# Performance work log

Hardware: AMD Instinct MI355X
Metric: run time of the kernel (lower is better)

The kernel has to match this reference:

```python
import jax, jax.numpy as jnp
import numpy as np

S = 8        # parallel streams (encoder/decoder pairs)
T_ENC = 12   # encoder timesteps per stream
H = 256      # hidden size
F = 316      # input features
B = 1024     # batch
MAX_LEN = 48
SCALE = 1.0 / np.sqrt(H).astype(np.float32)  # MHA single-head scaling


def _lstm_gates_to_hc(gates, c):
    # PyTorch gate order: i, f, g, o
    i, f, g, o = jnp.split(gates, 4, axis=-1)
    c_new = jax.nn.sigmoid(f) * c + jax.nn.sigmoid(i) * jnp.tanh(g)
    h_new = jax.nn.sigmoid(o) * jnp.tanh(c_new)
    return h_new, c_new


def setup_inputs() -> dict:
    key = jax.random.key(0)
    ks = jax.random.split(key, 20)
    w = 0.05
    inp = {
        'x': jax.random.normal(ks[0], (B, 96, F), jnp.float32),
        'tgt': jax.random.normal(ks[1], (B, MAX_LEN), jnp.float32),
        # encoder LSTM (per-stream stacked): input F -> H
        'W_ih_e': jax.random.normal(ks[2], (S, 4 * H, F), jnp.float32) * w,
        'W_hh_e': jax.random.normal(ks[3], (S, 4 * H, H), jnp.float32) * w,
        'b_ih_e': jnp.zeros((S, 4 * H), jnp.float32),
        'b_hh_e': jnp.zeros((S, 4 * H), jnp.float32),
        # decoder LSTM: input 1 -> H
        'W_ih_d': jax.random.normal(ks[4], (S, 4 * H, 1), jnp.float32) * w,
        'W_hh_d': jax.random.normal(ks[5], (S, 4 * H, H), jnp.float32) * w,
        'b_ih_d': jnp.zeros((S, 4 * H), jnp.float32),
        'b_hh_d': jnp.zeros((S, 4 * H), jnp.float32),
        # MultiheadAttention: in_proj [3H,H] per stream, out_proj [H,H]
        'W_in_attn': jax.random.normal(ks[6], (S, 3 * H, H), jnp.float32) * w,
        'b_in_attn': jnp.zeros((S, 3 * H), jnp.float32),
        'W_out_attn': jax.random.normal(ks[7], (S, H, H), jnp.float32) * w,
        'b_out_attn': jnp.zeros((S, H), jnp.float32),
        # decoder out_fc: 2H -> 1
        'W_fcout': jax.random.normal(ks[8], (S, 1, 2 * H), jnp.float32) * w,
        'b_fcout': jnp.zeros((S, 1), jnp.float32),
        # final fc: 8 -> 1
        'W_fc': jax.random.normal(ks[9], (1, S), jnp.float32) * w,
        'b_fc': jnp.zeros((1,), jnp.float32),
    }
    return inp


def _forward(x, tgt, W_ih_e, W_hh_e, b_ih_e, b_hh_e,
             W_ih_d, W_hh_d, b_ih_d, b_hh_d,
             W_in_attn, b_in_attn, W_out_attn, b_out_attn,
             W_fcout, b_fcout, W_fc, b_fc):
    batch, max_len = x.shape[0], tgt.shape[1]
    # time-major then split 96 steps into 8 streams of 12: [S, T_ENC, B, F]
    xe = x.transpose(1, 0, 2).reshape(S, T_ENC, batch, F)

    # ---- encoders: batched LSTM over 8 streams ----
    def enc_step(carry, xt):  # xt [S,B,F]
        h, c = carry
        gates = (jnp.einsum('sbf,sgf->sbg', xt, W_ih_e) + b_ih_e[:, None, :]
                 + jnp.einsum('sbh,sgh->sbg', h, W_hh_e) + b_hh_e[:, None, :])
        h, c = _lstm_gates_to_hc(gates, c)
        return (h, c), h

    h0 = jnp.zeros((S, batch, H), x.dtype)
    (hT, cT), enc_out = jax.lax.scan(enc_step, (h0, h0), xe.transpose(1, 0, 2, 3))
    # enc_out: [T_ENC, S, B, H]; (hT, cT) seed the decoder hidden state

    # ---- precompute attention K,V ----
    Wq, Wk, Wv = jnp.split(W_in_attn, 3, axis=1)  # each [S,H,H]
    bq, bk, bv = jnp.split(b_in_attn, 3, axis=1)  # each [S,H]
    k = jnp.einsum('tsbh,seh->tsbe', enc_out, Wk) + bk[None, :, None, :]
    v = jnp.einsum('tsbh,seh->tsbe', enc_out, Wv) + bv[None, :, None, :]

    # teacher-forced decoder inputs: step 0 uses x[-1,:,0], step t uses tgt[:,t-1]
    inputs = jnp.concatenate([x[:, -1, 0][None, :], tgt.T[:-1]], axis=0)  # [L,B]

    def dec_step(carry, inp):  # inp [B]
        h, c = carry
        it = jnp.broadcast_to(inp[None, :, None], (S, h.shape[1], 1))
        gates = (jnp.einsum('sbi,sgi->sbg', it, W_ih_d) + b_ih_d[:, None, :]
                 + jnp.einsum('sbh,sgh->sbg', h, W_hh_d) + b_hh_d[:, None, :])
        h, c = _lstm_gates_to_hc(gates, c)
        # single-query MHA (1 head) against encoder outputs
        q = jnp.einsum('sbh,seh->sbe', h, Wq) + bq[:, None, :]
        scores = jnp.einsum('sbe,tsbe->sbt', q, k) * SCALE
        attn = jax.nn.softmax(scores, axis=-1)
        ctx = jnp.einsum('sbt,tsbe->sbe', attn, v)
        ctx = jnp.einsum('sbe,soe->sbo', ctx, W_out_attn) + b_out_attn[:, None, :]
        cat = jnp.concatenate([h, ctx], axis=-1)  # [S,B,2H]
        out = jnp.einsum('sbk,sok->sbo', cat, W_fcout) + b_fcout[:, None, :]
        return (h, c), out[..., 0]  # [S,B]

    _, outs = jax.lax.scan(dec_step, (hT, cT), inputs)  # [L,S,B]
    final = outs.transpose(0, 2, 1)                      # [L,B,S]
    y = jnp.einsum('lbs,os->lbo', final, W_fc) + b_fc    # [L,B,1]
    return y[..., 0].T                                    # [B,L]


def reference(x, tgt, W_ih_e, W_hh_e, b_ih_e, b_hh_e,
              W_ih_d, W_hh_d, b_ih_d, b_hh_d,
              W_in_attn, b_in_attn, W_out_attn, b_out_attn,
              W_fcout, b_fcout, W_fc, b_fc):
    return _forward(x, tgt, W_ih_e, W_hh_e, b_ih_e, b_hh_e,
                    W_ih_d, W_hh_d, b_ih_d, b_hh_d,
                    W_in_attn, b_in_attn, W_out_attn, b_out_attn,
                    W_fcout, b_fcout, W_fc, b_fc)
```

## Files before the change

### kernel.cpp

```cpp
#include <hip/hip_runtime.h>
#include <cstdio>
#include <cstdint>

#define S8     8
#define TENC   12
#define HDIM   256
#define FDIM   316
#define BATCH  1024
#define LDEC   48
#define DBT    32
#define KA     264
#define SCALE_ATTN 0.0625f

typedef short bf16x8 __attribute__((ext_vector_type(8)));
typedef float f32x4  __attribute__((ext_vector_type(4)));

__device__ __forceinline__ float sigf(float x) { return 1.0f / (1.0f + expf(-x)); }

__device__ __forceinline__ unsigned short f2bf(float f) {
  unsigned u = __builtin_bit_cast(unsigned, f);
  unsigned r = (u + 0x7fffu + ((u >> 16) & 1u)) >> 16;
  return (unsigned short)r;
}
__device__ __forceinline__ float bflo(unsigned u) {
  return __builtin_bit_cast(float, u << 16);
}
__device__ __forceinline__ float bfhi(unsigned u) {
  return __builtin_bit_cast(float, u & 0xffff0000u);
}

#define MFMA(acc, a, b) acc = __builtin_amdgcn_mfma_f32_16x16x32_bf16(a, b, acc, 0, 0, 0)

#define DOT8(a, q, hp) \
  a = fmaf(bflo(q.x), hp[0], a); a = fmaf(bfhi(q.x), hp[1], a); \
  a = fmaf(bflo(q.y), hp[2], a); a = fmaf(bfhi(q.y), hp[3], a); \
  a = fmaf(bflo(q.z), hp[4], a); a = fmaf(bfhi(q.z), hp[5], a); \
  a = fmaf(bflo(q.w), hp[6], a); a = fmaf(bfhi(q.w), hp[7], a);

#define UNPS(dst, off, q) \
  dst[off+0] = bflo(q.x); dst[off+1] = bfhi(q.x); \
  dst[off+2] = bflo(q.y); dst[off+3] = bfhi(q.y); \
  dst[off+4] = bflo(q.z); dst[off+5] = bfhi(q.z); \
  dst[off+6] = bflo(q.w); dst[off+7] = bfhi(q.w);

__global__ __launch_bounds__(256) void transpose_k(const float* __restrict__ in,
                                                   float* __restrict__ out,
                                                   int R, int C) {
  __shared__ float tile[32][33];
  const int s = blockIdx.z;
  const size_t base = (size_t)s * R * C;
  const int r0 = blockIdx.y * 32, c0 = blockIdx.x * 32;
  const int tx = threadIdx.x & 31, ty = threadIdx.x >> 5;
  for (int i = ty; i < 32; i += 8) {
    int r = r0 + i, c = c0 + tx;
    if (r < R && c < C) tile[i][tx] = in[base + (size_t)r * C + c];
  }
  __syncthreads();
  for (int i = ty; i < 32; i += 8) {
    int c = c0 + i, r = r0 + tx;
    if (c < C && r < R) out[base + (size_t)c * R + r] = tile[tx][i];
  }
}

__global__ __launch_bounds__(256) void fold_gemm(const float* __restrict__ A, size_t sA,
                                                 const float* __restrict__ Bm, size_t sB,
                                                 float* __restrict__ out, size_t sO) {
  const int s = blockIdx.y, r0 = blockIdx.x * 32, col = threadIdx.x;
  A += (size_t)s * sA; Bm += (size_t)s * sB; out += (size_t)s * sO;
  float acc[32] = {};
  for (int e = 0; e < HDIM; ++e) {
    const float bvv = Bm[(size_t)e * HDIM + col];
#pragma unroll
    for (int r = 0; r < 32; ++r) acc[r] = fmaf(A[(size_t)e * HDIM + r0 + r], bvv, acc[r]);
  }
  for (int r = 0; r < 32; ++r) out[(size_t)(r0 + r) * HDIM + col] = acc[r];
}

__global__ __launch_bounds__(64) void pack_hl(const float* __restrict__ src, int Ksrc, int ksT,
                                              bf16x8* __restrict__ outhi,
                                              bf16x8* __restrict__ outlo) {
  const int s = blockIdx.z, ks = blockIdx.y, nt = blockIdx.x;
  const int lane = threadIdx.x, l15 = lane & 15, quad = lane >> 4;
  const int n = nt * 16 + l15, kb = ks * 32 + quad * 8;
  const float* row = src + ((size_t)s * 1024 + n) * Ksrc;
  union { bf16x8 v; unsigned short e[8]; } h, l;
#pragma unroll
  for (int j = 0; j < 8; ++j) {
    const int k = kb + j;
    const float v = (k < Ksrc) ? row[k] : 0.f;
    const unsigned short hi = f2bf(v);
    h.e[j] = hi;
    l.e[j] = f2bf(v - bflo(hi));
  }
  const size_t idx = (((size_t)s * ksT + ks) * 64 + nt) * 64 + lane;
  outhi[idx] = h.v;
  outlo[idx] = l.v;
}

__global__ __launch_bounds__(64) void pack_s(const float* __restrict__ src, int ntOff,
                                             bf16x8* __restrict__ out) {
  const int s = blockIdx.z, ks = blockIdx.y, nt = blockIdx.x;
  const int lane = threadIdx.x, l15 = lane & 15, quad = lane >> 4;
  const int n = nt * 16 + l15, kb = ks * 32 + quad * 8;
  const float* row = src + ((size_t)s * 256 + n) * 256;
  union { bf16x8 v; unsigned short e[8]; } h;
#pragma unroll
  for (int j = 0; j < 8; ++j) h.e[j] = f2bf(row[kb + j]);
  out[(((size_t)s * 8 + ks) * 32 + ntOff + nt) * 64 + lane] = h.v;
}

__global__ __launch_bounds__(256) void fold_vec2(const float* __restrict__ Win,
                                                 const float* __restrict__ bin,
                                                 const float* __restrict__ Wout,
                                                 const float* __restrict__ bout,
                                                 float* __restrict__ kbv,
                                                 float* __restrict__ cbias) {
  const int s = blockIdx.x, t = threadIdx.x;
  const float* bq = bin + s * 768;
  const float* bv = bin + s * 768 + 512;
  float a0 = 0.f, a1 = 0.f;
  for (int e = 0; e < 256; ++e) {
    a0 = fmaf(Win[((size_t)s * 768 + 256 + e) * 256 + t], bq[e], a0);
    a1 = fmaf(Wout[((size_t)s * 256 + t) * 256 + e], bv[e], a1);
  }
  kbv[s * 256 + t] = a0;
  cbias[s * 256 + t] = a1 + bout[s * 256 + t];
}

__global__ __launch_bounds__(256) void fold_mvw(const float* __restrict__ Mv,
                                                const float* __restrict__ Wfo,
                                                float* __restrict__ mvw) {
  const int s = blockIdx.x, k = threadIdx.x;
  float a = 0.f;
  for (int o = 0; o < 256; ++o)
    a = fmaf(Wfo[s * 512 + 256 + o], Mv[((size_t)s * 256 + o) * 256 + k], a);
  mvw[s * 256 + k] = a;
}

__global__ void fold_bias(const float* __restrict__ a, const float* __restrict__ b,
                          float* __restrict__ o, int n) {
  int i = blockIdx.x * 256 + threadIdx.x;
  if (i < n) o[i] = a[i] + b[i];
}

__global__ void build_decin(const float* __restrict__ x, const float* __restrict__ tgt,
                            float* __restrict__ dec_in) {
  int idx = blockIdx.x * 256 + threadIdx.x;
  if (idx >= LDEC * BATCH) return;
  int l = idx >> 10, b = idx & 1023;
  dec_in[idx] = (l == 0) ? x[(size_t)b * 96 * FDIM + 95 * FDIM]
                         : tgt[(size_t)b * LDEC + (l - 1)];
}

__global__ __launch_bounds__(512) void rec_phase(
    const float* __restrict__ x,
    const bf16x8* __restrict__ WxH, const bf16x8* __restrict__ WxL,
    const bf16x8* __restrict__ WeH, const bf16x8* __restrict__ WeL,
    const bf16x8* __restrict__ WdH, const bf16x8* __restrict__ WdL,
    const float* __restrict__ be, const float* __restrict__ bd,
    const float* __restrict__ wihd, const float* __restrict__ Wfo,
    const float* __restrict__ decin,
    unsigned* __restrict__ hEnc,
    unsigned short* __restrict__ hDec,
    float* __restrict__ hdPart)
{
  __shared__ unsigned short hAhi[DBT * KA];
  __shared__ unsigned short hAlo[DBT * KA];
  __shared__ float beS[1024];
  __shared__ float bdS[1024];
  __shared__ float wdS[1024];
  __shared__ float wfoS[256];
  __shared__ float scrR[DBT * 8];

  const int bid = blockIdx.x;
  const int s = bid & 7, b0 = (bid >> 3) * DBT;
  const int tid = threadIdx.x;
  const int w = tid >> 6, lane = tid & 63, l15 = lane & 15, quad = lane >> 4;

  for (int i = tid; i < DBT * KA; i += 512) { hAhi[i] = 0; hAlo[i] = 0; }
  for (int i = tid; i < 1024; i += 512) {
    beS[i] = be[s * 1024 + i];
    bdS[i] = bd[s * 1024 + i];
    wdS[i] = wihd[s * 1024 + i];
  }
  if (tid < 256) wfoS[tid] = Wfo[s * 512 + tid];

  float cst[2][2][4];
#pragma unroll
  for (int a = 0; a < 2; ++a)
#pragma unroll
    for (int b = 0; b < 2; ++b)
#pragma unroll
      for (int r = 0; r < 4; ++r) cst[a][b][r] = 0.f;

  const bf16x8* wxh = WxH + (size_t)s * 10 * 64 * 64;
  const bf16x8* wxl = WxL + (size_t)s * 10 * 64 * 64;
  const bf16x8* weh = WeH + (size_t)s * 8 * 64 * 64;
  const bf16x8* wel = WeL + (size_t)s * 8 * 64 * 64;
  const bf16x8* wdh = WdH + (size_t)s * 8 * 64 * 64;
  const bf16x8* wdl = WdL + (size_t)s * 8 * 64 * 64;

  __syncthreads();

  for (int t = 0; t < TENC; ++t) {
    f32x4 acc[2][2][4];
#pragma unroll
    for (int mt = 0; mt < 2; ++mt)
#pragma unroll
      for (int st = 0; st < 2; ++st)
#pragma unroll
        for (int c = 0; c < 4; ++c) acc[mt][st][c] = (f32x4){0.f, 0.f, 0.f, 0.f};

    const size_t xoff = (size_t)(s * TENC + t) * FDIM;
    for (int ks = 0; ks < 10; ++ks) {
      bf16x8 axh[2], axl[2];
#pragma unroll
      for (int mt = 0; mt < 2; ++mt) {
        const f32x4* xr = (const f32x4*)(x + (size_t)(b0 + 16 * mt + l15) * (96 * FDIM)
                                         + xoff + ks * 32 + quad * 8);
        const f32x4 v0 = __builtin_nontemporal_load(xr);
        f32x4 v1;
        if (ks == 9 && quad == 3) v1 = (f32x4){0.f, 0.f, 0.f, 0.f};
        else v1 = __builtin_nontemporal_load(xr + 1);
        float vv[8];
#pragma unroll
        for (int j = 0; j < 4; ++j) { vv[j] = v0[j]; vv[4 + j] = v1[j]; }
        union { bf16x8 v; unsigned short e[8]; } uh, ul;
#pragma unroll
        for (int j = 0; j < 8; ++j) {
          const unsigned short hi = f2bf(vv[j]);
          uh.e[j] = hi;
          ul.e[j] = f2bf(vv[j] - bflo(hi));
        }
        axh[mt] = uh.v; axl[mt] = ul.v;
      }
#pragma unroll
      for (int st = 0; st < 2; ++st)
#pragma unroll
        for (int c = 0; c < 4; ++c) {
          const int nt = c * 16 + 2 * w + st;
          const bf16x8 bh = wxh[(ks * 64 + nt) * 64 + lane];
          const bf16x8 bl = wxl[(ks * 64 + nt) * 64 + lane];
          MFMA(acc[0][st][c], axh[0], bh); MFMA(acc[0][st][c], axh[0], bl); MFMA(acc[0][st][c], axl[0], bh);
          MFMA(acc[1][st][c], axh[1], bh); MFMA(acc[1][st][c], axh[1], bl); MFMA(acc[1][st][c], axl[1], bh);
        }
    }
#pragma unroll 2
    for (int ks = 0; ks < 8; ++ks) {
      bf16x8 ah[2], al[2];
#pragma unroll
      for (int mt = 0; mt < 2; ++mt) {
        const int ao = (16 * mt + l15) * KA + ks * 32 + quad * 8;
        ah[mt] = *(const bf16x8*)&hAhi[ao];
        al[mt] = *(const bf16x8*)&hAlo[ao];
      }
#pragma unroll
      for (int st = 0; st < 2; ++st)
#pragma unroll
        for (int c = 0; c < 4; ++c) {
          const int nt = c * 16 + 2 * w + st;
          const bf16x8 bh = weh[(ks * 64 + nt) * 64 + lane];
          const bf16x8 bl = wel[(ks * 64 + nt) * 64 + lane];
          MFMA(acc[0][st][c], ah[0], bh); MFMA(acc[0][st][c], ah[0], bl); MFMA(acc[0][st][c], al[0], bh);
          MFMA(acc[1][st][c], ah[1], bh); MFMA(acc[1][st][c], ah[1], bl); MFMA(acc[1][st][c], al[1], bh);
        }
    }
    float hv[2][2][4];
#pragma unroll
    for (int st = 0; st < 2; ++st) {
      const int J0 = 32 * w + 16 * st + l15;
      const float g0 = beS[J0];
      const float g1 = beS[256 + J0];
      const float g2 = beS[512 + J0];
      const float g3 = beS[768 + J0];
#pragma unroll
      for (int mt = 0; mt < 2; ++mt)
#pragma unroll
        for (int reg = 0; reg < 4; ++reg) {
          const float gi = sigf(acc[mt][st][0][reg] + g0);
          const float gf = sigf(acc[mt][st][1][reg] + g1);
          const float gg = tanhf(acc[mt][st][2][reg] + g2);
          const float go = sigf(acc[mt][st][3][reg] + g3);
          const float cn = fmaf(gf, cst[mt][st][reg], gi * gg);
          cst[mt][st][reg] = cn;
          hv[mt][st][reg] = go * tanhf(cn);
        }
    }
    __syncthreads();
#pragma unroll
    for (int mt = 0; mt < 2; ++mt)
#pragma unroll
      for (int st = 0; st < 2; ++st)
#pragma unroll
        for (int reg = 0; reg < 4; ++reg) {
          const int R = 16 * mt + 4 * quad + reg;
          const int J = 32 * w + 16 * st + l15;
          const float v = hv[mt][st][reg];
          const unsigned short hi = f2bf(v);
          const unsigned short lo = f2bf(v - bflo(hi));
          hAhi[R * KA + J] = hi;
          hAlo[R * KA + J] = lo;
          __builtin_nontemporal_store((unsigned)hi | ((unsigned)lo << 16),
              &hEnc[((size_t)(t * S8 + s) * BATCH + b0 + R) * HDIM + J]);
        }
    __syncthreads();
  }

  for (int l = 0; l < LDEC; ++l) {
    f32x4 acc[2][2][4];
#pragma unroll
    for (int mt = 0; mt < 2; ++mt)
#pragma unroll
      for (int st = 0; st < 2; ++st)
#pragma unroll
        for (int c = 0; c < 4; ++c) acc[mt][st][c] = (f32x4){0.f, 0.f, 0.f, 0.f};

#pragma unroll 2
    for (int ks = 0; ks < 8; ++ks) {
      bf16x8 ah[2], al[2];
#pragma unroll
      for (int mt = 0; mt < 2; ++mt) {
        const int ao = (16 * mt + l15) * KA + ks * 32 + quad * 8;
        ah[mt] = *(const bf16x8*)&hAhi[ao];
        al[mt] = *(const bf16x8*)&hAlo[ao];
      }
#pragma unroll
      for (int st = 0; st < 2; ++st)
#pragma unroll
        for (int c = 0; c < 4; ++c) {
          const int nt = c * 16 + 2 * w + st;
          const bf16x8 bh = wdh[(ks * 64 + nt) * 64 + lane];
          const bf16x8 bl = wdl[(ks * 64 + nt) * 64 + lane];
          MFMA(acc[0][st][c], ah[0], bh); MFMA(acc[0][st][c], ah[0], bl); MFMA(acc[0][st][c], al[0], bh);
          MFMA(acc[1][st][c], ah[1], bh); MFMA(acc[1][st][c], ah[1], bl); MFMA(acc[1][st][c], al[1], bh);
        }
    }
    float hv[2][2][4];
#pragma unroll
    for (int st = 0; st < 2; ++st) {
      const int J0 = 32 * w + 16 * st + l15;
      const float b0g = bdS[J0];
      const float b1g = bdS[256 + J0];
      const float b2g = bdS[512 + J0];
      const float b3g = bdS[768 + J0];
      const float w0g = wdS[J0];
      const float w1g = wdS[256 + J0];
      const float w2g = wdS[512 + J0];
      const float w3g = wdS[768 + J0];
#pragma unroll
      for (int mt = 0; mt < 2; ++mt)
#pragma unroll
        for (int reg = 0; reg < 4; ++reg) {
          const int R = 16 * mt + 4 * quad + reg;
          const float it = decin[(size_t)l * BATCH + b0 + R];
          const float gi = sigf(fmaf(it, w0g, acc[mt][st][0][reg] + b0g));
          const float gf = sigf(fmaf(it, w1g, acc[mt][st][1][reg] + b1g));
          const float gg = tanhf(fmaf(it, w2g, acc[mt][st][2][reg] + b2g));
          const float go = sigf(fmaf(it, w3g, acc[mt][st][3][reg] + b3g));
          const float cn = fmaf(gf, cst[mt][st][reg], gi * gg);
          cst[mt][st][reg] = cn;
          hv[mt][st][reg] = go * tanhf(cn);
        }
    }
    __syncthreads();
#pragma unroll
    for (int mt = 0; mt < 2; ++mt)
#pragma unroll
      for (int st = 0; st < 2; ++st)
#pragma unroll
        for (int reg = 0; reg < 4; ++reg) {
          const int R = 16 * mt + 4 * quad + reg;
          const int J = 32 * w + 16 * st + l15;
          const float v = hv[mt][st][reg];
          const unsigned short hi = f2bf(v);
          hAhi[R * KA + J] = hi;
          hAlo[R * KA + J] = f2bf(v - bflo(hi));
          __builtin_nontemporal_store(hi,
              &hDec[((size_t)(l * S8 + s) * BATCH + b0 + R) * HDIM + J]);
        }
    {
      float part[8];
#pragma unroll
      for (int mt = 0; mt < 2; ++mt)
#pragma unroll
        for (int reg = 0; reg < 4; ++reg) {
          const int J0 = 32 * w + l15;
          part[mt * 4 + reg] = hv[mt][0][reg] * wfoS[J0] + hv[mt][1][reg] * wfoS[J0 + 16];
        }
#pragma unroll
      for (int i = 0; i < 8; ++i) {
        float v = part[i];
        v += __shfl_xor(v, 1, 16);
        v += __shfl_xor(v, 2, 16);
        v += __shfl_xor(v, 4, 16);
        v += __shfl_xor(v, 8, 16);
        part[i] = v;
      }
      if (l15 == 0) {
#pragma unroll
        for (int mt = 0; mt < 2; ++mt)
#pragma unroll
          for (int reg = 0; reg < 4; ++reg)
            scrR[(16 * mt + 4 * quad + reg) * 8 + w] = part[mt * 4 + reg];
      }
    }
    __syncthreads();
    if (tid < DBT) {
      float a = 0.f;
#pragma unroll
      for (int p = 0; p < 8; ++p) a += scrR[tid * 8 + p];
      hdPart[((size_t)l * S8 + s) * BATCH + b0 + tid] = a;
    }
  }
}

__global__ __launch_bounds__(256) void attn_phase(
    const unsigned* __restrict__ hEnc, const unsigned short* __restrict__ hDec,
    const bf16x8* __restrict__ AMvF,
    const float* __restrict__ kbv, const float* __restrict__ cbias,
    const float* __restrict__ mvw,
    const float* __restrict__ Wfo, const float* __restrict__ bfo,
    const float* __restrict__ hdPart,
    float* __restrict__ douts)
{
  __shared__ unsigned short kpL[TENC][16][KA];
  __shared__ float scr[16 * TENC * 17];
  __shared__ float sc[16][TENC];
  __shared__ float kbs[TENC][16];
  __shared__ float vw[TENC][16];

  const int s = blockIdx.y, b0 = blockIdx.x * 16;
  const int tid = threadIdx.x;
  const int w = tid >> 6, lane = tid & 63, l15 = lane & 15, quad = lane >> 4;

  const bf16x8* amv = AMvF + (size_t)s * 8 * 32 * 64;
  const float* kvv = kbv + s * 256;
  const float* mvv = mvw + s * 256;
  const float* cbs = cbias + s * 256;
  const float* wfo = Wfo + s * 512;
  const float bfos = bfo[s];

  float cw = 0.f;
  for (int e = 0; e < 256; ++e) cw = fmaf(cbs[e], wfo[256 + e], cw);

  for (int t = 0; t < TENC; ++t) {
    f32x4 acc[4];
#pragma unroll
    for (int c = 0; c < 4; ++c) acc[c] = (f32x4){0.f, 0.f, 0.f, 0.f};
    for (int ks = 0; ks < 8; ++ks) {
      const unsigned* hp = hEnc + ((size_t)(t * S8 + s) * BATCH + b0 + l15) * HDIM
                         + ks * 32 + quad * 8;
      union { bf16x8 v; unsigned short e[8]; } uh, ul;
#pragma unroll
      for (int j = 0; j < 8; ++j) {
        const unsigned u = hp[j];
        uh.e[j] = (unsigned short)u;
        ul.e[j] = (unsigned short)(u >> 16);
      }
#pragma unroll
      for (int c = 0; c < 4; ++c) {
        const int nt = w * 4 + c;
        const bf16x8 b = amv[(ks * 32 + nt) * 64 + lane];
        MFMA(acc[c], uh.v, b); MFMA(acc[c], ul.v, b);
      }
    }
#pragma unroll
    for (int c = 0; c < 4; ++c)
#pragma unroll
      for (int reg = 0; reg < 4; ++reg)
        kpL[t][4 * quad + reg][(w * 4 + c) * 16 + l15] = f2bf(acc[c][reg]);
  }
  for (int t = 0; t < TENC; ++t) {
    const int row = tid >> 4, p = tid & 15;
    const unsigned* hp = hEnc + ((size_t)(t * S8 + s) * BATCH + b0 + row) * HDIM + p * 16;
    float a = 0.f, b = 0.f;
#pragma unroll
    for (int k = 0; k < 16; ++k) {
      const unsigned u = hp[k];
      const float h = bflo(u) + bfhi(u);
      a = fmaf(kvv[p * 16 + k], h, a);
      b = fmaf(mvv[p * 16 + k], h, b);
    }
    scr[row * 34 + p] = a;
    scr[row * 34 + 17 + p] = b;
    __syncthreads();
    if (tid < 16) {
      float sa = 0.f, sb = 0.f;
#pragma unroll
      for (int p2 = 0; p2 < 16; ++p2) { sa += scr[tid * 34 + p2]; sb += scr[tid * 34 + 17 + p2]; }
      kbs[t][tid] = sa;
      vw[t][tid] = sb;
    }
    __syncthreads();
  }

  for (int l = 0; l < LDEC; ++l) {
    const int row = tid & 15, pp = tid >> 4;
    float hh[16];
    {
      const unsigned short* hp = hDec + ((size_t)(l * S8 + s) * BATCH + b0 + row) * HDIM + pp * 16;
      const uint4 q0 = *(const uint4*)hp;
      const uint4 q1 = *(const uint4*)(hp + 8);
      UNPS(hh, 0, q0);
      UNPS(hh, 8, q1);
    }
#pragma unroll 2
    for (int t = 0; t < TENC; ++t) {
      const uint4 q0 = *(const uint4*)&kpL[t][row][pp * 16];
      const uint4 q1 = *(const uint4*)&kpL[t][row][pp * 16 + 8];
      float a = 0.f;
      { const float* hp8 = &hh[0]; DOT8(a, q0, hp8); }
      { const float* hp8 = &hh[8]; DOT8(a, q1, hp8); }
      scr[(row * TENC + t) * 17 + pp] = a;
    }
    __syncthreads();
    if (tid < 192) {
      const int r2 = tid & 15, t2 = tid >> 4;
      float a = kbs[t2][r2];
#pragma unroll
      for (int p2 = 0; p2 < 16; ++p2) a += scr[(r2 * TENC + t2) * 17 + p2];
      sc[r2][t2] = a * SCALE_ATTN;
    }
    __syncthreads();
    if (tid < 16) {
      float m = sc[tid][0];
#pragma unroll
      for (int t2 = 1; t2 < TENC; ++t2) m = fmaxf(m, sc[tid][t2]);
      float e[TENC], sum = 0.f;
#pragma unroll
      for (int t2 = 0; t2 < TENC; ++t2) { e[t2] = expf(sc[tid][t2] - m); sum += e[t2]; }
      const float inv = 1.0f / sum;
      float av = 0.f;
#pragma unroll
      for (int t2 = 0; t2 < TENC; ++t2) av = fmaf(e[t2] * inv, vw[t2][tid], av);
      const float hd = hdPart[((size_t)l * S8 + s) * BATCH + b0 + tid];
      douts[((size_t)l * S8 + s) * BATCH + b0 + tid] = hd + av + cw + bfos;
    }
    __syncthreads();
  }
}

__global__ void final_fc(const float* __restrict__ douts, const float* __restrict__ Wfc,
                         const float* __restrict__ bfc, float* __restrict__ out) {
  int idx = blockIdx.x * 256 + threadIdx.x;
  if (idx >= BATCH * LDEC) return;
  int b = idx / LDEC, l = idx - b * LDEC;
  float a = bfc[0];
#pragma unroll
  for (int s = 0; s < S8; ++s)
    a = fmaf(douts[((size_t)l * S8 + s) * BATCH + b], Wfc[s], a);
  out[idx] = a;
}

extern "C" void kernel_launch(void* const* d_in, const int* in_sizes, int n_in,
                              void* d_out, int out_size, void* d_ws, size_t ws_size,
                              hipStream_t stream) {
  const float* x          = (const float*)d_in[0];
  const float* tgt        = (const float*)d_in[1];
  const float* W_ih_e     = (const float*)d_in[2];
  const float* W_hh_e     = (const float*)d_in[3];
  const float* b_ih_e     = (const float*)d_in[4];
  const float* b_hh_e     = (const float*)d_in[5];
  const float* W_ih_d     = (const float*)d_in[6];
  const float* W_hh_d     = (const float*)d_in[7];
  const float* b_ih_d     = (const float*)d_in[8];
  const float* b_hh_d     = (const float*)d_in[9];
  const float* W_in_attn  = (const float*)d_in[10];
  const float* b_in_attn  = (const float*)d_in[11];
  const float* W_out_attn = (const float*)d_in[12];
  const float* b_out_attn = (const float*)d_in[13];
  const float* W_fcout    = (const float*)d_in[14];
  const float* b_fcout    = (const float*)d_in[15];
  const float* W_fc       = (const float*)d_in[16];
  const float* b_fc       = (const float*)d_in[17];

  char* wsb = (char*)d_ws;
  size_t off = 0;
  auto alloc = [&](size_t bytes) {
    void* p = wsb + off; off += (bytes + 255) & ~(size_t)255; return p;
  };
  float*  douts = (float*)alloc((size_t)LDEC * S8 * BATCH * 4);
  float*  decin = (float*)alloc((size_t)LDEC * BATCH * 4);
  float*  hdPart= (float*)alloc((size_t)LDEC * S8 * BATCH * 4);
  float*  Pmat  = (float*)alloc((size_t)S8 * 256 * 256 * 4);
  float*  Mvmat = (float*)alloc((size_t)S8 * 256 * 256 * 4);
  float*  WoT   = (float*)alloc((size_t)S8 * 256 * 256 * 4);
  bf16x8* WxH   = (bf16x8*)alloc((size_t)S8 * 10 * 64 * 64 * 16);
  bf16x8* WxL   = (bf16x8*)alloc((size_t)S8 * 10 * 64 * 64 * 16);
  bf16x8* WeH   = (bf16x8*)alloc((size_t)S8 * 8 * 64 * 64 * 16);
  bf16x8* WeL   = (bf16x8*)alloc((size_t)S8 * 8 * 64 * 64 * 16);
  bf16x8* WdH   = (bf16x8*)alloc((size_t)S8 * 8 * 64 * 64 * 16);
  bf16x8* WdL   = (bf16x8*)alloc((size_t)S8 * 8 * 64 * 64 * 16);
  bf16x8* AMvF  = (bf16x8*)alloc((size_t)S8 * 8 * 32 * 64 * 16);
  float*  kbv   = (float*)alloc((size_t)S8 * 256 * 4);
  float*  cbias = (float*)alloc((size_t)S8 * 256 * 4);
  float*  mvw   = (float*)alloc((size_t)S8 * 256 * 4);
  float*  beF   = (float*)alloc((size_t)S8 * 1024 * 4);
  float*  bdF   = (float*)alloc((size_t)S8 * 1024 * 4);
  unsigned* hEnc = (unsigned*)alloc((size_t)TENC * S8 * BATCH * HDIM * 4);
  unsigned short* hDec = (unsigned short*)alloc((size_t)LDEC * S8 * BATCH * HDIM * 2);
  if (off > ws_size) {
    fprintf(stderr, "kernel_launch: ws too small: need %zu bytes, have %zu\n", off, ws_size);
    return;
  }

  transpose_k<<<dim3(8, 8, S8), 256, 0, stream>>>(W_out_attn, WoT, 256, 256);
  fold_gemm<<<dim3(8, S8), 256, 0, stream>>>(W_in_attn, (size_t)768 * 256,
                                             W_in_attn + 256 * 256, (size_t)768 * 256,
                                             Pmat, (size_t)256 * 256);
  fold_gemm<<<dim3(8, S8), 256, 0, stream>>>(WoT, (size_t)256 * 256,
                                             W_in_attn + 2 * 256 * 256, (size_t)768 * 256,
                                             Mvmat, (size_t)256 * 256);
  pack_hl<<<dim3(64, 10, S8), 64, 0, stream>>>(W_ih_e, FDIM, 10, WxH, WxL);
  pack_hl<<<dim3(64, 8, S8), 64, 0, stream>>>(W_hh_e, 256, 8, WeH, WeL);
  pack_hl<<<dim3(64, 8, S8), 64, 0, stream>>>(W_hh_d, 256, 8, WdH, WdL);
  pack_s<<<dim3(16, 8, S8), 64, 0, stream>>>(Pmat, 0, AMvF);
  fold_vec2<<<S8, 256, 0, stream>>>(W_in_attn, b_in_attn, W_out_attn, b_out_attn, kbv, cbias);
  fold_mvw<<<S8, 256, 0, stream>>>(Mvmat, W_fcout, mvw);
  fold_bias<<<(S8 * 1024 + 255) / 256, 256, 0, stream>>>(b_ih_e, b_hh_e, beF, S8 * 1024);
  fold_bias<<<(S8 * 1024 + 255) / 256, 256, 0, stream>>>(b_ih_d, b_hh_d, bdF, S8 * 1024);
  build_decin<<<(LDEC * BATCH + 255) / 256, 256, 0, stream>>>(x, tgt, decin);

  rec_phase<<<256, 512, 0, stream>>>(
      x, WxH, WxL, WeH, WeL, WdH, WdL, beF, bdF, W_ih_d, W_fcout, decin,
      hEnc, hDec, hdPart);

  attn_phase<<<dim3(64, S8), 256, 0, stream>>>(
      hEnc, hDec, AMvF, kbv, cbias, mvw, W_fcout, b_fcout, hdPart, douts);

  final_fc<<<(BATCH * LDEC + 255) / 256, 256, 0, stream>>>(douts, W_fc, b_fc, (float*)d_out);
}
```

Before: 2.741 ms.

## Widen attention kernel to 1024 threads and process two decoder steps per iteration

The attention kernel grows from 256 to 1024 threads per block. Each of the 16 waves now computes one key-projection MFMA tile instead of four per wave, and the kbs/vw reductions use wave shuffles instead of shared-memory passes. The decoder loop handles two decoder steps at once, one per half-block, with each thread doing an 8-element dot product. This is meant to raise parallelism and cut the number of loop iterations and barriers in a latency-bound kernel, at the cost of more threads per block, which may limit occupancy.

```diff
diff --git a/kernel.cpp b/kernel.cpp
--- a/kernel.cpp
+++ b/kernel.cpp
@@ -414,7 +414,7 @@
   }
 }
 
-__global__ __launch_bounds__(256) void attn_phase(
+__global__ __launch_bounds__(1024) void attn_phase(
     const unsigned* __restrict__ hEnc, const unsigned short* __restrict__ hDec,
     const bf16x8* __restrict__ AMvF,
     const float* __restrict__ kbv, const float* __restrict__ cbias,
@@ -424,8 +424,8 @@
     float* __restrict__ douts)
 {
   __shared__ unsigned short kpL[TENC][16][KA];
-  __shared__ float scr[16 * TENC * 17];
-  __shared__ float sc[16][TENC];
+  __shared__ float scr2[2 * 16 * TENC * 33];
+  __shared__ float sc[2][16][TENC];
   __shared__ float kbs[TENC][16];
   __shared__ float vw[TENC][16];
 
@@ -444,9 +444,7 @@
   for (int e = 0; e < 256; ++e) cw = fmaf(cbs[e], wfo[256 + e], cw);
 
   for (int t = 0; t < TENC; ++t) {
-    f32x4 acc[4];
-#pragma unroll
-    for (int c = 0; c < 4; ++c) acc[c] = (f32x4){0.f, 0.f, 0.f, 0.f};
+    f32x4 acc = (f32x4){0.f, 0.f, 0.f, 0.f};
     for (int ks = 0; ks < 8; ++ks) {
       const unsigned* hp = hEnc + ((size_t)(t * S8 + s) * BATCH + b0 + l15) * HDIM
                          + ks * 32 + quad * 8;
@@ -457,84 +455,78 @@
         uh.e[j] = (unsigned short)u;
         ul.e[j] = (unsigned short)(u >> 16);
       }
-#pragma unroll
-      for (int c = 0; c < 4; ++c) {
-        const int nt = w * 4 + c;
-        const bf16x8 b = amv[(ks * 32 + nt) * 64 + lane];
-        MFMA(acc[c], uh.v, b); MFMA(acc[c], ul.v, b);
-      }
-    }
-#pragma unroll
-    for (int c = 0; c < 4; ++c)
-#pragma unroll
-      for (int reg = 0; reg < 4; ++reg)
-        kpL[t][4 * quad + reg][(w * 4 + c) * 16 + l15] = f2bf(acc[c][reg]);
-  }
-  for (int t = 0; t < TENC; ++t) {
-    const int row = tid >> 4, p = tid & 15;
-    const unsigned* hp = hEnc + ((size_t)(t * S8 + s) * BATCH + b0 + row) * HDIM + p * 16;
-    float a = 0.f, b = 0.f;
-#pragma unroll
-    for (int k = 0; k < 16; ++k) {
-      const unsigned u = hp[k];
-      const float h = bflo(u) + bfhi(u);
-      a = fmaf(kvv[p * 16 + k], h, a);
-      b = fmaf(mvv[p * 16 + k], h, b);
-    }
-    scr[row * 34 + p] = a;
-    scr[row * 34 + 17 + p] = b;
-    __syncthreads();
-    if (tid < 16) {
-      float sa = 0.f, sb = 0.f;
-#pragma unroll
-      for (int p2 = 0; p2 < 16; ++p2) { sa += scr[tid * 34 + p2]; sb += scr[tid * 34 + 17 + p2]; }
-      kbs[t][tid] = sa;
-      vw[t][tid] = sb;
-    }
-    __syncthreads();
-  }
-
-  for (int l = 0; l < LDEC; ++l) {
-    const int row = tid & 15, pp = tid >> 4;
-    float hh[16];
+      const bf16x8 b = amv[(ks * 32 + w) * 64 + lane];
+      MFMA(acc, uh.v, b); MFMA(acc, ul.v, b);
+    }
+#pragma unroll
+    for (int reg = 0; reg < 4; ++reg)
+      kpL[t][4 * quad + reg][w * 16 + l15] = f2bf(acc[reg]);
+  }
+
+  {
+    const int row = tid >> 6;
+    const int p = lane;
+    for (int t = 0; t < TENC; ++t) {
+      const unsigned* hp = hEnc + ((size_t)(t * S8 + s) * BATCH + b0 + row) * HDIM + p * 4;
+      float a = 0.f, bv = 0.f;
+#pragma unroll
+      for (int j = 0; j < 4; ++j) {
+        const unsigned u = hp[j];
+        const float h = bflo(u) + bfhi(u);
+        a = fmaf(kvv[p * 4 + j], h, a);
+        bv = fmaf(mvv[p * 4 + j], h, bv);
+      }
+#pragma unroll
+      for (int off = 1; off < 64; off <<= 1) {
+        a += __shfl_xor(a, off, 64);
+        bv += __shfl_xor(bv, off, 64);
+      }
+      if (lane == 0) { kbs[t][row] = a; vw[t][row] = bv; }
+    }
+  }
+  __syncthreads();
+
+  for (int li = 0; li < LDEC / 2; ++li) {
+    const int lh = tid >> 9;
+    const int l = li * 2 + lh;
+    const int t2 = tid & 511;
+    const int row = t2 & 15, pp = t2 >> 4;
+    float hh[8];
     {
-      const unsigned short* hp = hDec + ((size_t)(l * S8 + s) * BATCH + b0 + row) * HDIM + pp * 16;
-      const uint4 q0 = *(const uint4*)hp;
-      const uint4 q1 = *(const uint4*)(hp + 8);
-      UNPS(hh, 0, q0);
-      UNPS(hh, 8, q1);
+      const unsigned short* hp = hDec + ((size_t)(l * S8 + s) * BATCH + b0 + row) * HDIM + pp * 8;
+      const uint4 q = *(const uint4*)hp;
+      UNPS(hh, 0, q);
     }
 #pragma unroll 2
     for (int t = 0; t < TENC; ++t) {
-      const uint4 q0 = *(const uint4*)&kpL[t][row][pp * 16];
-      const uint4 q1 = *(const uint4*)&kpL[t][row][pp * 16 + 8];
+      const uint4 q0 = *(const uint4*)&kpL[t][row][pp * 8];
       float a = 0.f;
-      { const float* hp8 = &hh[0]; DOT8(a, q0, hp8); }
-      { const float* hp8 = &hh[8]; DOT8(a, q1, hp8); }
-      scr[(row * TENC + t) * 17 + pp] = a;
+      const float* hp8 = hh;
+      DOT8(a, q0, hp8);
+      scr2[((lh * 16 + row) * TENC + t) * 33 + pp] = a;
     }
     __syncthreads();
-    if (tid < 192) {
-      const int r2 = tid & 15, t2 = tid >> 4;
-      float a = kbs[t2][r2];
-#pragma unroll
-      for (int p2 = 0; p2 < 16; ++p2) a += scr[(r2 * TENC + t2) * 17 + p2];
-      sc[r2][t2] = a * SCALE_ATTN;
+    if (t2 < 192) {
+      const int r2 = t2 & 15, tt = t2 >> 4;
+      float a = kbs[tt][r2];
+#pragma unroll
+      for (int p2 = 0; p2 < 32; ++p2) a += scr2[((lh * 16 + r2) * TENC + tt) * 33 + p2];
+      sc[lh][r2][tt] = a * SCALE_ATTN;
     }
     __syncthreads();
-    if (tid < 16) {
-      float m = sc[tid][0];
-#pragma unroll
-      for (int t2 = 1; t2 < TENC; ++t2) m = fmaxf(m, sc[tid][t2]);
+    if (t2 < 16) {
+      float m = sc[lh][t2][0];
+#pragma unroll
+      for (int tt = 1; tt < TENC; ++tt) m = fmaxf(m, sc[lh][t2][tt]);
       float e[TENC], sum = 0.f;
 #pragma unroll
-      for (int t2 = 0; t2 < TENC; ++t2) { e[t2] = expf(sc[tid][t2] - m); sum += e[t2]; }
+      for (int tt = 0; tt < TENC; ++tt) { e[tt] = expf(sc[lh][t2][tt] - m); sum += e[tt]; }
       const float inv = 1.0f / sum;
       float av = 0.f;
 #pragma unroll
-      for (int t2 = 0; t2 < TENC; ++t2) av = fmaf(e[t2] * inv, vw[t2][tid], av);
-      const float hd = hdPart[((size_t)l * S8 + s) * BATCH + b0 + tid];
-      douts[((size_t)l * S8 + s) * BATCH + b0 + tid] = hd + av + cw + bfos;
+      for (int tt = 0; tt < TENC; ++tt) av = fmaf(e[tt] * inv, vw[tt][t2], av);
+      const float hd = hdPart[((size_t)l * S8 + s) * BATCH + b0 + t2];
+      douts[((size_t)l * S8 + s) * BATCH + b0 + t2] = hd + av + cw + bfos;
     }
     __syncthreads();
   }
@@ -625,7 +617,7 @@
       x, WxH, WxL, WeH, WeL, WdH, WdL, beF, bdF, W_ih_d, W_fcout, decin,
       hEnc, hDec, hdPart);
 
-  attn_phase<<<dim3(64, S8), 256, 0, stream>>>(
+  attn_phase<<<dim3(64, S8), 1024, 0, stream>>>(
       hEnc, hDec, AMvF, kbv, cbias, mvw, W_fcout, b_fcout, hdPart, douts);
 
   final_fc<<<(BATCH * LDEC + 255) / 256, 256, 0, stream>>>(douts, W_fc, b_fc, (float*)d_out);
```

New measurement: 2.713 ms. No clear change (-1.0%).
